# Kernel tuning notes

Hardware: AMD Instinct MI355X
Metric: run time of the kernel (lower is better)

## Reference

```python
import jax, jax.numpy as jnp
import numpy as np

N = 100000      # nodes
E = 1600000     # edges (avg degree 16)
F_IN = 256      # num_features
H2 = 128        # nhid * 2 (layer 1 width)
H = 64          # nhid (layer 2 width)
C = 10          # num_classes


def setup_inputs() -> dict:
    key = jax.random.key(0)
    ks = jax.random.split(key, 8)
    x = jax.random.normal(ks[0], (N, F_IN), dtype=jnp.float32)
    edge_index = jax.random.randint(ks[1], (2, E), 0, N, dtype=jnp.int64)
    W1 = jax.random.normal(ks[2], (F_IN, H2), dtype=jnp.float32) / np.float32(np.sqrt(F_IN))
    b1 = jnp.zeros((H2,), jnp.float32)
    W2 = jax.random.normal(ks[3], (H2, H), dtype=jnp.float32) / np.float32(np.sqrt(H2))
    b2 = jnp.zeros((H,), jnp.float32)
    Wl = jax.random.normal(ks[4], (H, C), dtype=jnp.float32) / np.float32(np.sqrt(H))
    bl = jnp.zeros((C,), jnp.float32)
    return {"x": x, "edge_index": edge_index, "W1": W1, "b1": b1,
            "W2": W2, "b2": b2, "Wl": Wl, "bl": bl}


def reference(x, edge_index, W1, b1, W2, b2, Wl, bl):
    # --- GCN normalization with self-loops (PyG GCNConv default) ---
    loops = jnp.arange(N, dtype=edge_index.dtype)
    src = jnp.concatenate([edge_index[0], loops])  # message sources
    dst = jnp.concatenate([edge_index[1], loops])  # message targets
    deg = jax.ops.segment_sum(jnp.ones(src.shape[0], x.dtype), dst, num_segments=N)
    dinv = jnp.where(deg > 0, jax.lax.rsqrt(deg), 0.0)
    norm = dinv[src] * dinv[dst]                   # [E+N]

    def gcn_conv(h, W, b):
        m = h @ W                                  # transform first (out_channels small)
        agg = jax.ops.segment_sum(m[src] * norm[:, None], dst, num_segments=N)
        return agg + b

    h = jax.nn.relu(gcn_conv(x, W1, b1))           # [N, H2]
    h = jax.nn.relu(gcn_conv(h, W2, b2))           # [N, H]
    logits = h @ Wl + bl                            # [N, C]
    return jax.nn.log_softmax(logits, axis=-1)
```

## Files before the change

### kernel.cpp

```cpp
#include <hip/hip_runtime.h>


typedef unsigned short ushort_t;
typedef unsigned int uint_t;
typedef __attribute__((ext_vector_type(8))) short short8;
typedef __attribute__((ext_vector_type(4))) float floatx4;

static __device__ __forceinline__ ushort_t f2bf(float f) {
    union { float f; uint_t u; } c; c.f = f;
    return (ushort_t)((c.u + 0x8000u) >> 16);
}
static __device__ __forceinline__ float bf2f(ushort_t h) {
    union { uint_t u; float f; } c; c.u = ((uint_t)h) << 16;
    return c.f;
}
static __device__ __forceinline__ float2 up2(uint_t p) {
    union { uint_t u; float f; } lo, hi;
    lo.u = p << 16; hi.u = p & 0xffff0000u;
    return make_float2(lo.f, hi.f);
}
static __device__ __forceinline__ uint_t pk2bf(float a, float b) {
    return ((uint_t)f2bf(b) << 16) | (uint_t)f2bf(a);
}
static __device__ __forceinline__ void ld_lds16(void* lds, const void* g) {
    __builtin_amdgcn_global_load_lds(
        (const __attribute__((address_space(1))) unsigned int*)g,
        (__attribute__((address_space(3))) unsigned int*)lds, 16, 0, 0);
}

#define NBMAX 800
#define ECAP  4096

__global__ __launch_bounds__(256) void hist_kernel(
    const int* __restrict__ dst, int* __restrict__ histG, int E, int NB) {
    __shared__ int h[NBMAX];
    for (int i = threadIdx.x; i < NB; i += 256) h[i] = 0;
    __syncthreads();
    int i16 = (blockIdx.x * 256 + threadIdx.x) * 16;
    if (i16 + 15 < E) {
        #pragma unroll
        for (int u = 0; u < 4; u++) {
            int4 d = *(const int4*)(dst + i16 + u * 4);
            atomicAdd(&h[d.x >> 7], 1);
            atomicAdd(&h[d.y >> 7], 1);
            atomicAdd(&h[d.z >> 7], 1);
            atomicAdd(&h[d.w >> 7], 1);
        }
    } else {
        for (int e = i16; e < E; e++) atomicAdd(&h[dst[e] >> 7], 1);
    }
    __syncthreads();
    int* out = histG + (size_t)blockIdx.x * NB;
    for (int i = threadIdx.x; i < NB; i += 256) out[i] = h[i];
}

__global__ __launch_bounds__(256) void scan_bucket(
    int* __restrict__ histG, int* __restrict__ totG, int GB, int NB) {
    int b = blockIdx.x * 256 + threadIdx.x;
    if (b >= NB) return;
    int run = 0;
    int g = 0;
    for (; g + 16 <= GB; g += 16) {
        int vv[16];
        #pragma unroll
        for (int u = 0; u < 16; u++) vv[u] = histG[(size_t)(g + u) * NB + b];
        #pragma unroll
        for (int u = 0; u < 16; u++) {
            histG[(size_t)(g + u) * NB + b] = run;
            run += vv[u];
        }
    }
    for (; g < GB; g++) {
        int v = histG[(size_t)g * NB + b];
        histG[(size_t)g * NB + b] = run;
        run += v;
    }
    totG[b] = run;
}

__global__ void scan_tot(const int* __restrict__ totG, int* __restrict__ bbase,
                         int NB) {
    __shared__ int s[256];
    const int t = threadIdx.x;
    int running = 0;
    int nch = (NB + 255) / 256;
    for (int c = 0; c < nch; c++) {
        int j = c * 256 + t;
        int v = (j < NB) ? totG[j] : 0;
        s[t] = v;
        __syncthreads();
        for (int off = 1; off < 256; off <<= 1) {
            int tmp = (t >= off) ? s[t - off] : 0;
            __syncthreads();
            s[t] += tmp;
            __syncthreads();
        }
        if (j < NB) bbase[j] = s[t] - v + running;
        int ctot = s[255];
        __syncthreads();
        running += ctot;
    }
    if (t == 0) bbase[NB] = running;
}

__global__ __launch_bounds__(256) void scatter_kernel(
    const int* __restrict__ src, const int* __restrict__ dst,
    const int* __restrict__ histG, const int* __restrict__ bbase,
    int* __restrict__ packed, int E, int NB) {
    __shared__ int lbase[NBMAX];
    const int* row = histG + (size_t)blockIdx.x * NB;
    for (int i = threadIdx.x; i < NB; i += 256)
        lbase[i] = bbase[i] + row[i];
    __syncthreads();
    int i16 = (blockIdx.x * 256 + threadIdx.x) * 16;
    if (i16 + 15 < E) {
        #pragma unroll
        for (int u = 0; u < 4; u++) {
            int4 s4 = *(const int4*)(src + i16 + u * 4);
            int4 d4 = *(const int4*)(dst + i16 + u * 4);
            int p;
            p = atomicAdd(&lbase[d4.x >> 7], 1); packed[p] = s4.x | ((d4.x & 127) << 17);
            p = atomicAdd(&lbase[d4.y >> 7], 1); packed[p] = s4.y | ((d4.y & 127) << 17);
            p = atomicAdd(&lbase[d4.z >> 7], 1); packed[p] = s4.z | ((d4.z & 127) << 17);
            p = atomicAdd(&lbase[d4.w >> 7], 1); packed[p] = s4.w | ((d4.w & 127) << 17);
        }
    } else {
        for (int e = i16; e < E; e++) {
            int d = dst[e];
            int p = atomicAdd(&lbase[d >> 7], 1);
            packed[p] = src[e] | ((d & 127) << 17);
        }
    }
}

__global__ __launch_bounds__(256) void bucket_csr(
    const int* __restrict__ packed, const int* __restrict__ bbase,
    int* __restrict__ rowptr, int* __restrict__ csr,
    float* __restrict__ dinv, int N, int NB) {
    __shared__ int ebuf[ECAP];
    __shared__ int cnt[128];
    __shared__ int pl[128];
    __shared__ int s[256];
    const int b = blockIdx.x;
    const int t = threadIdx.x;
    const int lo = bbase[b];
    const int hi = bbase[b + 1];
    int m = hi - lo;
    if (m > ECAP) m = ECAP;
    for (int i = t; i < m; i += 256) ebuf[i] = packed[lo + i];
    if (t < 128) cnt[t] = 0;
    __syncthreads();
    for (int i = t; i < m; i += 256) atomicAdd(&cnt[ebuf[i] >> 17], 1);
    __syncthreads();
    const int node0 = b << 7;
    int c = (t < 128) ? cnt[t] : 0;
    if (t < 128 && node0 + t < N)
        dinv[node0 + t] = rsqrtf((float)(c + 1));
    s[t] = c;
    __syncthreads();
    for (int off = 1; off < 256; off <<= 1) {
        int tmp = (t >= off) ? s[t - off] : 0;
        __syncthreads();
        s[t] += tmp;
        __syncthreads();
    }
    int excl = s[t] - c;
    if (t < 128) {
        pl[t] = excl;
        if (node0 + t <= N) rowptr[node0 + t] = lo + excl;
    }
    __syncthreads();
    for (int i = t; i < m; i += 256) {
        int e = ebuf[i];
        int p = atomicAdd(&pl[e >> 17], 1);
        csr[lo + p] = e & 0x1FFFF;
    }
}

__global__ void wcvt2_kernel(const float* __restrict__ W1, const float* __restrict__ W2,
                             ushort_t* __restrict__ W1t, ushort_t* __restrict__ W2t) {
    int i = blockIdx.x * 256 + threadIdx.x;
    if (i < 256 * 128) {
        int k = i / 128, n = i % 128;
        W1t[n * 256 + k] = f2bf(W1[i]);
    }
    int j = i - 256 * 128;
    if (j >= 0 && j < 128 * 64) {
        int k = j / 64, n = j % 64;
        W2t[n * 128 + k] = f2bf(W2[j]);
    }
}

__global__ __launch_bounds__(256) void gemm1_mfma(
    const float* __restrict__ A, const ushort_t* __restrict__ Bt,
    const float* __restrict__ dinv, ushort_t* __restrict__ out, int M) {
    __shared__ float    As[64 * 256];
    __shared__ ushort_t Bs[128 * 256];
    const int tid = threadIdx.x;
    const int l = tid & 63;
    const int wave = tid >> 6;
    const int lrow = l & 15, hh = l >> 4;
    const int m0 = blockIdx.x * 64;

    #pragma unroll
    for (int rd = 0; rd < 16; rd++) {
        int idx = rd * 256 + tid;
        int r = idx >> 6, cs = idx & 63;
        int row = m0 + r; if (row >= M) row = M - 1;
        int cl = cs ^ (r & 7);
        ld_lds16(&As[idx * 4], A + (size_t)row * 256 + cl * 4);
    }
    #pragma unroll
    for (int rd = 0; rd < 16; rd++) {
        int idx = rd * 256 + tid;
        int n = idx >> 5, cs = idx & 31;
        int cl = cs ^ (n & 7);
        ld_lds16(&Bs[idx * 8], Bt + (size_t)n * 256 + cl * 8);
    }
    __syncthreads();

    floatx4 acc[8];
    #pragma unroll
    for (int nt = 0; nt < 8; nt++)
        acc[nt] = (floatx4){0.f, 0.f, 0.f, 0.f};

    const int wr = wave * 16 + lrow;
    #pragma unroll
    for (int kk = 0; kk < 8; kk++) {
        int c0 = kk * 8 + hh * 2;
        float4 u = *(const float4*)&As[wr * 256 + ((c0    ) ^ (wr & 7)) * 4];
        float4 v = *(const float4*)&As[wr * 256 + ((c0 + 1) ^ (wr & 7)) * 4];
        short8 afr;
        afr[0] = (short)f2bf(u.x); afr[1] = (short)f2bf(u.y);
        afr[2] = (short)f2bf(u.z); afr[3] = (short)f2bf(u.w);
        afr[4] = (short)f2bf(v.x); afr[5] = (short)f2bf(v.y);
        afr[6] = (short)f2bf(v.z); afr[7] = (short)f2bf(v.w);
        short8 bfr[8];
        #pragma unroll
        for (int nt = 0; nt < 8; nt++) {
            int n = nt * 16 + lrow;
            int c = kk * 4 + hh;
            bfr[nt] = *(const short8*)&Bs[n * 256 + (c ^ (n & 7)) * 8];
        }
        #pragma unroll
        for (int nt = 0; nt < 8; nt++)
            acc[nt] = __builtin_amdgcn_mfma_f32_16x16x32_bf16(
                afr, bfr[nt], acc[nt], 0, 0, 0);
    }

    const int mbase = m0 + wave * 16 + hh * 4;
    float4 dv = *(const float4*)&dinv[mbase];
    float d[4] = {dv.x, dv.y, dv.z, dv.w};
    #pragma unroll
    for (int i = 0; i < 4; i++) {
        int m = mbase + i;
        if (m < M) {
            #pragma unroll
            for (int nt = 0; nt < 8; nt++)
                out[(size_t)m * 128 + nt * 16 + lrow] =
                    f2bf(acc[nt][i] * d[i]);
        }
    }
}

__global__ __launch_bounds__(256) void gemm2_mfma(
    const ushort_t* __restrict__ A, const ushort_t* __restrict__ Bt,
    const float* __restrict__ dinv, ushort_t* __restrict__ out, int M) {
    __shared__ ushort_t As[64 * 128];
    __shared__ ushort_t Bs[64 * 128];
    const int tid = threadIdx.x;
    const int l = tid & 63;
    const int wave = tid >> 6;
    const int lrow = l & 15, hh = l >> 4;
    const int m0 = blockIdx.x * 64;

    #pragma unroll
    for (int rd = 0; rd < 4; rd++) {
        int idx = rd * 256 + tid;
        int r = idx >> 4, cs = idx & 15;
        int row = m0 + r; if (row >= M) row = M - 1;
        int cl = cs ^ (r & 7);
        ld_lds16(&As[idx * 8], A + (size_t)row * 128 + cl * 8);
    }
    #pragma unroll
    for (int rd = 0; rd < 4; rd++) {
        int idx = rd * 256 + tid;
        int n = idx >> 4, cs = idx & 15;
        int cl = cs ^ (n & 7);
        ld_lds16(&Bs[idx * 8], Bt + (size_t)n * 128 + cl * 8);
    }
    __syncthreads();

    floatx4 acc[4];
    #pragma unroll
    for (int nt = 0; nt < 4; nt++)
        acc[nt] = (floatx4){0.f, 0.f, 0.f, 0.f};

    const int wr = wave * 16 + lrow;
    #pragma unroll
    for (int kk = 0; kk < 4; kk++) {
        int c0 = kk * 4 + hh;
        short8 afr = *(const short8*)&As[wr * 128 + (c0 ^ (wr & 7)) * 8];
        short8 bfr[4];
        #pragma unroll
        for (int nt = 0; nt < 4; nt++) {
            int n = nt * 16 + lrow;
            bfr[nt] = *(const short8*)&Bs[n * 128 + (c0 ^ (n & 7)) * 8];
        }
        #pragma unroll
        for (int nt = 0; nt < 4; nt++)
            acc[nt] = __builtin_amdgcn_mfma_f32_16x16x32_bf16(
                afr, bfr[nt], acc[nt], 0, 0, 0);
    }

    const int mbase = m0 + wave * 16 + hh * 4;
    float4 dv = *(const float4*)&dinv[mbase];
    float d[4] = {dv.x, dv.y, dv.z, dv.w};
    #pragma unroll
    for (int i = 0; i < 4; i++) {
        int m = mbase + i;
        if (m < M) {
            #pragma unroll
            for (int nt = 0; nt < 4; nt++)
                out[(size_t)m * 64 + nt * 16 + lrow] =
                    f2bf(acc[nt][i] * d[i]);
        }
    }
}

__global__ __launch_bounds__(256) void spmm_relu128(
    const ushort_t* __restrict__ Mm, const int* __restrict__ rowptr,
    const int* __restrict__ csr, const float* __restrict__ dinv,
    const float* __restrict__ bias, ushort_t* __restrict__ out, int n, int doff) {
    int v = (blockIdx.x * 256 + threadIdx.x) >> 6;
    int lane = threadIdx.x & 63;
    if (v >= n) return;
    int jb = rowptr[v];
    int cntn = rowptr[v + 1] - jb;
    const char* Mb = (const char*)Mm;
    const int slot = lane >> 4;
    const int q = lane & 15;
    const uint_t qb = (uint_t)q * 16;

    float2 a0 = {0.f, 0.f}, a1 = a0, a2 = a0, a3 = a0;
    if (slot == 0) {
        uint4 s = *(const uint4*)(Mb + ((size_t)v << 8) + qb);
        a0 = up2(s.x); a1 = up2(s.y); a2 = up2(s.z); a3 = up2(s.w);
    }

    for (int base = 0; base < cntn; base += 64) {
        int m = cntn - base; if (m > 64) m = 64;
        int roff = (base + lane < cntn) ? (csr[jb + base + lane] << 8) : doff;
        int m4 = (m + 3) & ~3;
        int jj = 0;
        for (; jj + 16 <= m4; jj += 16) {
            uint_t o[4];
            #pragma unroll
            for (int t = 0; t < 4; t++)
                o[t] = (uint_t)__shfl(roff, jj + 4 * t + slot) + qb;
            uint4 p[4];
            #pragma unroll
            for (int t = 0; t < 4; t++) p[t] = *(const uint4*)(Mb + o[t]);
            #pragma unroll
            for (int t = 0; t < 4; t++) {
                float2 f;
                f = up2(p[t].x); a0.x += f.x; a0.y += f.y;
                f = up2(p[t].y); a1.x += f.x; a1.y += f.y;
                f = up2(p[t].z); a2.x += f.x; a2.y += f.y;
                f = up2(p[t].w); a3.x += f.x; a3.y += f.y;
            }
        }
        for (; jj < m4; jj += 4) {
            uint_t o = (uint_t)__shfl(roff, jj + slot) + qb;
            uint4 p = *(const uint4*)(Mb + o);
            float2 f;
            f = up2(p.x); a0.x += f.x; a0.y += f.y;
            f = up2(p.y); a1.x += f.x; a1.y += f.y;
            f = up2(p.z); a2.x += f.x; a2.y += f.y;
            f = up2(p.w); a3.x += f.x; a3.y += f.y;
        }
    }
    float r[8] = {a0.x, a0.y, a1.x, a1.y, a2.x, a2.y, a3.x, a3.y};
    #pragma unroll
    for (int i = 0; i < 8; i++) r[i] += __shfl_xor(r[i], 16);
    #pragma unroll
    for (int i = 0; i < 8; i++) r[i] += __shfl_xor(r[i], 32);
    if (slot == 0) {
        float d = dinv[v];
        float4 bv0 = *(const float4*)&bias[q * 8];
        float4 bv1 = *(const float4*)&bias[q * 8 + 4];
        float o0 = fmaxf(d * r[0] + bv0.x, 0.f);
        float o1 = fmaxf(d * r[1] + bv0.y, 0.f);
        float o2 = fmaxf(d * r[2] + bv0.z, 0.f);
        float o3 = fmaxf(d * r[3] + bv0.w, 0.f);
        float o4 = fmaxf(d * r[4] + bv1.x, 0.f);
        float o5 = fmaxf(d * r[5] + bv1.y, 0.f);
        float o6 = fmaxf(d * r[6] + bv1.z, 0.f);
        float o7 = fmaxf(d * r[7] + bv1.w, 0.f);
        uint4 pk;
        pk.x = pk2bf(o0, o1); pk.y = pk2bf(o2, o3);
        pk.z = pk2bf(o4, o5); pk.w = pk2bf(o6, o7);
        *(uint4*)(out + (size_t)v * 128 + q * 8) = pk;
    }
}

__global__ __launch_bounds__(256) void spmm_relu64(
    const ushort_t* __restrict__ Mm, const int* __restrict__ rowptr,
    const int* __restrict__ csr, const float* __restrict__ dinv,
    const float* __restrict__ bias, ushort_t* __restrict__ out, int n, int doff) {
    int v = (blockIdx.x * 256 + threadIdx.x) >> 6;
    int lane = threadIdx.x & 63;
    if (v >= n) return;
    int jb = rowptr[v];
    int cntn = rowptr[v + 1] - jb;
    const char* Mb = (const char*)Mm;
    const int slot = lane >> 3;
    const int q = lane & 7;
    const uint_t qb = (uint_t)q * 16;

    float2 a0 = {0.f, 0.f}, a1 = a0, a2 = a0, a3 = a0;
    if (slot == 0) {
        uint4 s = *(const uint4*)(Mb + ((size_t)v << 7) + qb);
        a0 = up2(s.x); a1 = up2(s.y); a2 = up2(s.z); a3 = up2(s.w);
    }

    for (int base = 0; base < cntn; base += 64) {
        int m = cntn - base; if (m > 64) m = 64;
        int roff = (base + lane < cntn) ? (csr[jb + base + lane] << 7) : doff;
        int m8 = (m + 7) & ~7;
        int jj = 0;
        for (; jj + 16 <= m8; jj += 16) {
            uint_t o[2];
            #pragma unroll
            for (int t = 0; t < 2; t++)
                o[t] = (uint_t)__shfl(roff, jj + 8 * t + slot) + qb;
            uint4 p[2];
            #pragma unroll
            for (int t = 0; t < 2; t++) p[t] = *(const uint4*)(Mb + o[t]);
            #pragma unroll
            for (int t = 0; t < 2; t++) {
                float2 f;
                f = up2(p[t].x); a0.x += f.x; a0.y += f.y;
                f = up2(p[t].y); a1.x += f.x; a1.y += f.y;
                f = up2(p[t].z); a2.x += f.x; a2.y += f.y;
                f = up2(p[t].w); a3.x += f.x; a3.y += f.y;
            }
        }
        for (; jj < m8; jj += 8) {
            uint_t o = (uint_t)__shfl(roff, jj + slot) + qb;
            uint4 p = *(const uint4*)(Mb + o);
            float2 f;
            f = up2(p.x); a0.x += f.x; a0.y += f.y;
            f = up2(p.y); a1.x += f.x; a1.y += f.y;
            f = up2(p.z); a2.x += f.x; a2.y += f.y;
            f = up2(p.w); a3.x += f.x; a3.y += f.y;
        }
    }
    float r[8] = {a0.x, a0.y, a1.x, a1.y, a2.x, a2.y, a3.x, a3.y};
    #pragma unroll
    for (int i = 0; i < 8; i++) r[i] += __shfl_xor(r[i], 8);
    #pragma unroll
    for (int i = 0; i < 8; i++) r[i] += __shfl_xor(r[i], 16);
    #pragma unroll
    for (int i = 0; i < 8; i++) r[i] += __shfl_xor(r[i], 32);
    if (slot == 0) {
        float d = dinv[v];
        float4 bv0 = *(const float4*)&bias[q * 8];
        float4 bv1 = *(const float4*)&bias[q * 8 + 4];
        float o0 = fmaxf(d * r[0] + bv0.x, 0.f);
        float o1 = fmaxf(d * r[1] + bv0.y, 0.f);
        float o2 = fmaxf(d * r[2] + bv0.z, 0.f);
        float o3 = fmaxf(d * r[3] + bv0.w, 0.f);
        float o4 = fmaxf(d * r[4] + bv1.x, 0.f);
        float o5 = fmaxf(d * r[5] + bv1.y, 0.f);
        float o6 = fmaxf(d * r[6] + bv1.z, 0.f);
        float o7 = fmaxf(d * r[7] + bv1.w, 0.f);
        uint4 pk;
        pk.x = pk2bf(o0, o1); pk.y = pk2bf(o2, o3);
        pk.z = pk2bf(o4, o5); pk.w = pk2bf(o6, o7);
        *(uint4*)(out + (size_t)v * 64 + q * 8) = pk;
    }
}

__global__ __launch_bounds__(256) void head_kernel(
    const ushort_t* __restrict__ h2, const float* __restrict__ Wl,
    const float* __restrict__ bl, float* __restrict__ out, int n) {
    __shared__ float Ws[64 * 10];
    __shared__ float bs[10];
    for (int i = threadIdx.x; i < 640; i += 256) Ws[i] = Wl[i];
    if (threadIdx.x < 10) bs[threadIdx.x] = bl[threadIdx.x];
    __syncthreads();
    int v = blockIdx.x * 256 + threadIdx.x;
    if (v >= n) return;
    float acc[10];
    #pragma unroll
    for (int c = 0; c < 10; c++) acc[c] = bs[c];
    const ushort_t* hrow = &h2[(size_t)v * 64];
    #pragma unroll
    for (int k0 = 0; k0 < 64; k0 += 8) {
        short8 hv = *(const short8*)&hrow[k0];
        #pragma unroll
        for (int kk = 0; kk < 8; kk++) {
            float hf = bf2f((ushort_t)hv[kk]);
            #pragma unroll
            for (int c = 0; c < 10; c++)
                acc[c] += hf * Ws[(k0 + kk) * 10 + c];
        }
    }
    float m = acc[0];
    #pragma unroll
    for (int c = 1; c < 10; c++) m = fmaxf(m, acc[c]);
    float s = 0.f;
    #pragma unroll
    for (int c = 0; c < 10; c++) s += expf(acc[c] - m);
    float lse = logf(s);
    #pragma unroll
    for (int c = 0; c < 10; c++) out[(size_t)v * 10 + c] = acc[c] - m - lse;
}

extern "C" void kernel_launch(void* const* d_in, const int* in_sizes, int n_in,
                              void* d_out, int out_size, void* d_ws, size_t ws_size,
                              hipStream_t stream) {
    const float* x   = (const float*)d_in[0];
    const int*   ei  = (const int*)d_in[1];
    const float* W1  = (const float*)d_in[2];
    const float* b1  = (const float*)d_in[3];
    const float* W2  = (const float*)d_in[4];
    const float* b2  = (const float*)d_in[5];
    const float* Wl  = (const float*)d_in[6];
    const float* bl  = (const float*)d_in[7];
    float*       out = (float*)d_out;

    const int N = in_sizes[0] / 256;
    const int E = in_sizes[1] / 2;
    const int* srcI = ei;
    const int* dstI = ei + E;

    const int NB = (N + 127) >> 7;
    const int GB = (E + 4095) / 4096;

    char* ws = (char*)d_ws;
    size_t off = 0;
    auto alloc = [&](size_t bytes) -> void* {
        void* p = ws + off;
        off = (off + bytes + 255) & ~(size_t)255;
        return p;
    };
    int*      histG  = (int*)alloc((size_t)GB * NB * 4);
    int*      totG   = (int*)alloc((size_t)NB * 4);
    int*      bbase  = (int*)alloc((size_t)(NB + 1) * 4);
    int*      packed = (int*)alloc((size_t)E * 4);
    int*      rowptr = (int*)alloc((size_t)(N + 1) * 4);
    float*    dinv   = (float*)alloc((size_t)(N + 128) * 4);
    int*      csr    = (int*)alloc((size_t)E * 4);
    ushort_t* W1t    = (ushort_t*)alloc((size_t)128 * 256 * 2);
    ushort_t* W2t    = (ushort_t*)alloc((size_t)64 * 128 * 2);
    ushort_t* bufA   = (ushort_t*)alloc((size_t)(N + 2) * 128 * 2);
    ushort_t* bufB   = (ushort_t*)alloc((size_t)N * 128 * 2);

    hist_kernel<<<GB, 256, 0, stream>>>(dstI, histG, E, NB);
    scan_bucket<<<(NB + 255) / 256, 256, 0, stream>>>(histG, totG, GB, NB);
    scan_tot<<<1, 256, 0, stream>>>(totG, bbase, NB);
    scatter_kernel<<<GB, 256, 0, stream>>>(srcI, dstI, histG, bbase, packed, E, NB);
    bucket_csr<<<NB, 256, 0, stream>>>(packed, bbase, rowptr, csr, dinv, N, NB);

    wcvt2_kernel<<<(256 * 128 + 128 * 64 + 255) / 256, 256, 0, stream>>>(W1, W2, W1t, W2t);

    const int gblk = (N + 63) / 64;
    gemm1_mfma<<<gblk, 256, 0, stream>>>(x, W1t, dinv, bufA, N);
    hipMemsetAsync(bufA + (size_t)N * 128, 0, 256, stream);
    spmm_relu128<<<(N + 3) / 4, 256, 0, stream>>>(bufA, rowptr, csr, dinv, b1, bufB, N, N << 8);
    gemm2_mfma<<<gblk, 256, 0, stream>>>(bufB, W2t, dinv, bufA, N);
    hipMemsetAsync(bufA + (size_t)N * 64, 0, 128, stream);
    spmm_relu64<<<(N + 3) / 4, 256, 0, stream>>>(bufA, rowptr, csr, dinv, b2, bufB, N, N << 7);
    head_kernel<<<(N + 255) / 256, 256, 0, stream>>>(bufB, Wl, bl, out, N);
}
```

Measured before the change: 361.6 us.

## Fuse small kernels: weight cvt into hist, scans, head into spmm64, drop memsets

Folds the weight bf16 conversion into extra blocks of the histogram kernel and merges the two scan kernels using a last-block-done atomic counter. The padding-row memsets are replaced by zero writes from the GEMM epilogues, and the final linear layer plus log-softmax is fused into the second SpMM via lane shuffles. This removes several kernel launches, two memsets and the round trip of the layer-2 activations through global memory. In exchange it adds atomic and fence overhead to the scan and a per-lane 8x10 FMA with shuffle reduction in the SpMM.

```diff
diff --git a/kernel.cpp b/kernel.cpp
--- a/kernel.cpp
+++ b/kernel.cpp
@@ -32,7 +32,24 @@
 #define ECAP  4096
 
 __global__ __launch_bounds__(256) void hist_kernel(
-    const int* __restrict__ dst, int* __restrict__ histG, int E, int NB) {
+    const int* __restrict__ dst, int* __restrict__ histG,
+    const float* __restrict__ W1, const float* __restrict__ W2,
+    ushort_t* __restrict__ W1t, ushort_t* __restrict__ W2t,
+    int* __restrict__ done, int E, int NB, int GB) {
+    if ((int)blockIdx.x >= GB) {
+        if ((int)blockIdx.x == GB && threadIdx.x == 0) *done = 0;
+        int i = ((int)blockIdx.x - GB) * 256 + threadIdx.x;
+        if (i < 256 * 128) {
+            int k = i / 128, n = i % 128;
+            W1t[n * 256 + k] = f2bf(W1[i]);
+        }
+        int j = i - 256 * 128;
+        if (j >= 0 && j < 128 * 64) {
+            int k = j / 64, n = j % 64;
+            W2t[n * 128 + k] = f2bf(W2[j]);
+        }
+        return;
+    }
     __shared__ int h[NBMAX];
     for (int i = threadIdx.x; i < NB; i += 256) h[i] = 0;
     __syncthreads();
@@ -50,57 +67,62 @@
         for (int e = i16; e < E; e++) atomicAdd(&h[dst[e] >> 7], 1);
     }
     __syncthreads();
-    int* out = histG + (size_t)blockIdx.x * NB;
-    for (int i = threadIdx.x; i < NB; i += 256) out[i] = h[i];
+    int* outp = histG + (size_t)blockIdx.x * NB;
+    for (int i = threadIdx.x; i < NB; i += 256) outp[i] = h[i];
 }
 
 __global__ __launch_bounds__(256) void scan_bucket(
-    int* __restrict__ histG, int* __restrict__ totG, int GB, int NB) {
+    int* __restrict__ histG, int* __restrict__ totG, int* __restrict__ bbase,
+    int* __restrict__ done, int GB, int NB, int nblk) {
+    __shared__ int isLast;
+    __shared__ int s[256];
     int b = blockIdx.x * 256 + threadIdx.x;
-    if (b >= NB) return;
-    int run = 0;
-    int g = 0;
-    for (; g + 16 <= GB; g += 16) {
-        int vv[16];
-        #pragma unroll
-        for (int u = 0; u < 16; u++) vv[u] = histG[(size_t)(g + u) * NB + b];
-        #pragma unroll
-        for (int u = 0; u < 16; u++) {
-            histG[(size_t)(g + u) * NB + b] = run;
-            run += vv[u];
-        }
-    }
-    for (; g < GB; g++) {
-        int v = histG[(size_t)g * NB + b];
-        histG[(size_t)g * NB + b] = run;
-        run += v;
-    }
-    totG[b] = run;
-}
-
-__global__ void scan_tot(const int* __restrict__ totG, int* __restrict__ bbase,
-                         int NB) {
-    __shared__ int s[256];
-    const int t = threadIdx.x;
+    if (b < NB) {
+        int run = 0;
+        int g = 0;
+        for (; g + 16 <= GB; g += 16) {
+            int vv[16];
+            #pragma unroll
+            for (int u = 0; u < 16; u++) vv[u] = histG[(size_t)(g + u) * NB + b];
+            #pragma unroll
+            for (int u = 0; u < 16; u++) {
+                histG[(size_t)(g + u) * NB + b] = run;
+                run += vv[u];
+            }
+        }
+        for (; g < GB; g++) {
+            int v = histG[(size_t)g * NB + b];
+            histG[(size_t)g * NB + b] = run;
+            run += v;
+        }
+        totG[b] = run;
+    }
+    __threadfence();
+    __syncthreads();
+    if (threadIdx.x == 0)
+        isLast = (atomicAdd(done, 1) == nblk - 1);
+    __syncthreads();
+    if (!isLast) return;
+    __threadfence();
     int running = 0;
     int nch = (NB + 255) / 256;
     for (int c = 0; c < nch; c++) {
-        int j = c * 256 + t;
+        int j = c * 256 + threadIdx.x;
         int v = (j < NB) ? totG[j] : 0;
-        s[t] = v;
+        s[threadIdx.x] = v;
         __syncthreads();
         for (int off = 1; off < 256; off <<= 1) {
-            int tmp = (t >= off) ? s[t - off] : 0;
+            int tmp = (threadIdx.x >= off) ? s[threadIdx.x - off] : 0;
             __syncthreads();
-            s[t] += tmp;
+            s[threadIdx.x] += tmp;
             __syncthreads();
         }
-        if (j < NB) bbase[j] = s[t] - v + running;
+        if (j < NB) bbase[j] = s[threadIdx.x] - v + running;
         int ctot = s[255];
         __syncthreads();
         running += ctot;
     }
-    if (t == 0) bbase[NB] = running;
+    if (threadIdx.x == 0) bbase[NB] = running;
 }
 
 __global__ __launch_bounds__(256) void scatter_kernel(
@@ -177,20 +199,6 @@
     }
 }
 
-__global__ void wcvt2_kernel(const float* __restrict__ W1, const float* __restrict__ W2,
-                             ushort_t* __restrict__ W1t, ushort_t* __restrict__ W2t) {
-    int i = blockIdx.x * 256 + threadIdx.x;
-    if (i < 256 * 128) {
-        int k = i / 128, n = i % 128;
-        W1t[n * 256 + k] = f2bf(W1[i]);
-    }
-    int j = i - 256 * 128;
-    if (j >= 0 && j < 128 * 64) {
-        int k = j / 64, n = j % 64;
-        W2t[n * 128 + k] = f2bf(W2[j]);
-    }
-}
-
 __global__ __launch_bounds__(256) void gemm1_mfma(
     const float* __restrict__ A, const ushort_t* __restrict__ Bt,
     const float* __restrict__ dinv, ushort_t* __restrict__ out, int M) {
@@ -259,6 +267,10 @@
             for (int nt = 0; nt < 8; nt++)
                 out[(size_t)m * 128 + nt * 16 + lrow] =
                     f2bf(acc[nt][i] * d[i]);
+        } else if (m == M) {
+            #pragma unroll
+            for (int nt = 0; nt < 8; nt++)
+                out[(size_t)M * 128 + nt * 16 + lrow] = 0;
         }
     }
 }
@@ -324,6 +336,10 @@
             for (int nt = 0; nt < 4; nt++)
                 out[(size_t)m * 64 + nt * 16 + lrow] =
                     f2bf(acc[nt][i] * d[i]);
+        } else if (m == M) {
+            #pragma unroll
+            for (int nt = 0; nt < 4; nt++)
+                out[(size_t)M * 64 + nt * 16 + lrow] = 0;
         }
     }
 }
@@ -404,10 +420,11 @@
     }
 }
 
-__global__ __launch_bounds__(256) void spmm_relu64(
+__global__ __launch_bounds__(256) void spmm64_head(
     const ushort_t* __restrict__ Mm, const int* __restrict__ rowptr,
     const int* __restrict__ csr, const float* __restrict__ dinv,
-    const float* __restrict__ bias, ushort_t* __restrict__ out, int n, int doff) {
+    const float* __restrict__ bias, const float* __restrict__ Wl,
+    const float* __restrict__ bl, float* __restrict__ out, int n, int doff) {
     int v = (blockIdx.x * 256 + threadIdx.x) >> 6;
     int lane = threadIdx.x & 63;
     if (v >= n) return;
@@ -467,55 +484,45 @@
         float d = dinv[v];
         float4 bv0 = *(const float4*)&bias[q * 8];
         float4 bv1 = *(const float4*)&bias[q * 8 + 4];
-        float o0 = fmaxf(d * r[0] + bv0.x, 0.f);
-        float o1 = fmaxf(d * r[1] + bv0.y, 0.f);
-        float o2 = fmaxf(d * r[2] + bv0.z, 0.f);
-        float o3 = fmaxf(d * r[3] + bv0.w, 0.f);
-        float o4 = fmaxf(d * r[4] + bv1.x, 0.f);
-        float o5 = fmaxf(d * r[5] + bv1.y, 0.f);
-        float o6 = fmaxf(d * r[6] + bv1.z, 0.f);
-        float o7 = fmaxf(d * r[7] + bv1.w, 0.f);
-        uint4 pk;
-        pk.x = pk2bf(o0, o1); pk.y = pk2bf(o2, o3);
-        pk.z = pk2bf(o4, o5); pk.w = pk2bf(o6, o7);
-        *(uint4*)(out + (size_t)v * 64 + q * 8) = pk;
-    }
-}
-
-__global__ __launch_bounds__(256) void head_kernel(
-    const ushort_t* __restrict__ h2, const float* __restrict__ Wl,
-    const float* __restrict__ bl, float* __restrict__ out, int n) {
-    __shared__ float Ws[64 * 10];
-    __shared__ float bs[10];
-    for (int i = threadIdx.x; i < 640; i += 256) Ws[i] = Wl[i];
-    if (threadIdx.x < 10) bs[threadIdx.x] = bl[threadIdx.x];
-    __syncthreads();
-    int v = blockIdx.x * 256 + threadIdx.x;
-    if (v >= n) return;
-    float acc[10];
-    #pragma unroll
-    for (int c = 0; c < 10; c++) acc[c] = bs[c];
-    const ushort_t* hrow = &h2[(size_t)v * 64];
-    #pragma unroll
-    for (int k0 = 0; k0 < 64; k0 += 8) {
-        short8 hv = *(const short8*)&hrow[k0];
-        #pragma unroll
-        for (int kk = 0; kk < 8; kk++) {
-            float hf = bf2f((ushort_t)hv[kk]);
+        float h[8];
+        h[0] = fmaxf(d * r[0] + bv0.x, 0.f);
+        h[1] = fmaxf(d * r[1] + bv0.y, 0.f);
+        h[2] = fmaxf(d * r[2] + bv0.z, 0.f);
+        h[3] = fmaxf(d * r[3] + bv0.w, 0.f);
+        h[4] = fmaxf(d * r[4] + bv1.x, 0.f);
+        h[5] = fmaxf(d * r[5] + bv1.y, 0.f);
+        h[6] = fmaxf(d * r[6] + bv1.z, 0.f);
+        h[7] = fmaxf(d * r[7] + bv1.w, 0.f);
+        float lg[10];
+        #pragma unroll
+        for (int c = 0; c < 10; c++) lg[c] = 0.f;
+        #pragma unroll
+        for (int i = 0; i < 8; i++) {
+            const float* wrow = &Wl[(q * 8 + i) * 10];
+            #pragma unroll
+            for (int c = 0; c < 10; c++) lg[c] += h[i] * wrow[c];
+        }
+        #pragma unroll
+        for (int c = 0; c < 10; c++) {
+            lg[c] += __shfl_xor(lg[c], 1);
+            lg[c] += __shfl_xor(lg[c], 2);
+            lg[c] += __shfl_xor(lg[c], 4);
+        }
+        if (q == 0) {
+            #pragma unroll
+            for (int c = 0; c < 10; c++) lg[c] += bl[c];
+            float mx = lg[0];
+            #pragma unroll
+            for (int c = 1; c < 10; c++) mx = fmaxf(mx, lg[c]);
+            float s = 0.f;
+            #pragma unroll
+            for (int c = 0; c < 10; c++) s += expf(lg[c] - mx);
+            float lse = logf(s);
             #pragma unroll
             for (int c = 0; c < 10; c++)
-                acc[c] += hf * Ws[(k0 + kk) * 10 + c];
-        }
-    }
-    float m = acc[0];
-    #pragma unroll
-    for (int c = 1; c < 10; c++) m = fmaxf(m, acc[c]);
-    float s = 0.f;
-    #pragma unroll
-    for (int c = 0; c < 10; c++) s += expf(acc[c] - m);
-    float lse = logf(s);
-    #pragma unroll
-    for (int c = 0; c < 10; c++) out[(size_t)v * 10 + c] = acc[c] - m - lse;
+                out[(size_t)v * 10 + c] = lg[c] - mx - lse;
+        }
+    }
 }
 
 extern "C" void kernel_launch(void* const* d_in, const int* in_sizes, int n_in,
@@ -538,6 +545,8 @@
 
     const int NB = (N + 127) >> 7;
     const int GB = (E + 4095) / 4096;
+    const int WB = (256 * 128 + 128 * 64 + 255) / 256;
+    const int SB = (NB + 255) / 256;
 
     char* ws = (char*)d_ws;
     size_t off = 0;
@@ -549,6 +558,7 @@
     int*      histG  = (int*)alloc((size_t)GB * NB * 4);
     int*      totG   = (int*)alloc((size_t)NB * 4);
     int*      bbase  = (int*)alloc((size_t)(NB + 1) * 4);
+    int*      done   = (int*)alloc(256);
     int*      packed = (int*)alloc((size_t)E * 4);
     int*      rowptr = (int*)alloc((size_t)(N + 1) * 4);
     float*    dinv   = (float*)alloc((size_t)(N + 128) * 4);
@@ -558,20 +568,16 @@
     ushort_t* bufA   = (ushort_t*)alloc((size_t)(N + 2) * 128 * 2);
     ushort_t* bufB   = (ushort_t*)alloc((size_t)N * 128 * 2);
 
-    hist_kernel<<<GB, 256, 0, stream>>>(dstI, histG, E, NB);
-    scan_bucket<<<(NB + 255) / 256, 256, 0, stream>>>(histG, totG, GB, NB);
-    scan_tot<<<1, 256, 0, stream>>>(totG, bbase, NB);
+    hist_kernel<<<GB + WB, 256, 0, stream>>>(dstI, histG, W1, W2, W1t, W2t,
+                                             done, E, NB, GB);
+    scan_bucket<<<SB, 256, 0, stream>>>(histG, totG, bbase, done, GB, NB, SB);
     scatter_kernel<<<GB, 256, 0, stream>>>(srcI, dstI, histG, bbase, packed, E, NB);
     bucket_csr<<<NB, 256, 0, stream>>>(packed, bbase, rowptr, csr, dinv, N, NB);
 
-    wcvt2_kernel<<<(256 * 128 + 128 * 64 + 255) / 256, 256, 0, stream>>>(W1, W2, W1t, W2t);
-
     const int gblk = (N + 63) / 64;
     gemm1_mfma<<<gblk, 256, 0, stream>>>(x, W1t, dinv, bufA, N);
-    hipMemsetAsync(bufA + (size_t)N * 128, 0, 256, stream);
     spmm_relu128<<<(N + 3) / 4, 256, 0, stream>>>(bufA, rowptr, csr, dinv, b1, bufB, N, N << 8);
     gemm2_mfma<<<gblk, 256, 0, stream>>>(bufB, W2t, dinv, bufA, N);
-    hipMemsetAsync(bufA + (size_t)N * 64, 0, 128, stream);
-    spmm_relu64<<<(N + 3) / 4, 256, 0, stream>>>(bufA, rowptr, csr, dinv, b2, bufB, N, N << 7);
-    head_kernel<<<(N + 255) / 256, 256, 0, stream>>>(bufB, Wl, bl, out, N);
-}
+    spmm64_head<<<(N + 3) / 4, 256, 0, stream>>>(bufA, rowptr, csr, dinv, b2,
+                                                 Wl, bl, out, N, N << 7);
+}
```

Result: slower. 404.3 us (+11.8%).
